# Optimization experiments

Hardware: AMD Instinct MI355X
Metric: run time of the kernel (lower is better)

The kernel has to match this reference:

```python
import jax, jax.numpy as jnp
import numpy as np

N = 100_000   # nodes
E = 1_600_000 # edges (avg degree 16)
D = 128       # input_dim
H = 128       # hidden_dim
G = 64        # graphs in batch
C = 2         # num_classes


def setup_inputs() -> dict:
    key = jax.random.key(0)
    ks = jax.random.split(key, 16)
    x = jax.random.normal(ks[0], (N, D), dtype=jnp.float32)
    edge_index = jax.random.randint(ks[1], (2, E), 0, N, dtype=jnp.int32)
    batch = jnp.sort(jax.random.randint(ks[2], (N,), 0, G, dtype=jnp.int32))
    def lin(k, fin, fout):
        s = 1.0 / np.sqrt(fin)
        kw, kb = jax.random.split(k)
        W = jax.random.uniform(kw, (fin, fout), jnp.float32, -s, s)
        b = jax.random.uniform(kb, (fout,), jnp.float32, -s, s)
        return W, b
    W0, b0 = lin(ks[3], D, H)
    W1, b1 = lin(ks[4], H, H)
    W2, b2 = lin(ks[5], H, H)
    Wc1, bc1 = lin(ks[6], 2 * H, H)
    Wc2, bc2 = lin(ks[7], H, C)
    return dict(x=x, edge_index=edge_index, batch=batch,
                W0=W0, b0=b0, W1=W1, b1=b1, W2=W2, b2=b2,
                Wc1=Wc1, bc1=bc1, Wc2=Wc2, bc2=bc2)


def _gcn_layer(x, W, b, src, dst, dinv):
    # GCNConv with self-loops and symmetric normalization:
    # out_i = sum_{j->i} d_j^{-1/2} d_i^{-1/2} (x_j W) + d_i^{-1} (x_i W) + b
    h = x @ W                                   # [N, H]
    coef = dinv[src] * dinv[dst]                # [E]
    agg = jax.ops.segment_sum(h[src] * coef[:, None], dst, num_segments=N)
    return agg + h * (dinv * dinv)[:, None] + b


def reference(x, edge_index, batch, W0, b0, W1, b1, W2, b2, Wc1, bc1, Wc2, bc2):
    src, dst = edge_index[0], edge_index[1]
    # degree with self-loops (in-degree on target nodes + 1)
    deg = jax.ops.segment_sum(jnp.ones((E,), jnp.float32), dst, num_segments=N) + 1.0
    dinv = jax.lax.rsqrt(deg)
    for W, b in ((W0, b0), (W1, b1), (W2, b2)):
        x = jax.nn.relu(_gcn_layer(x, W, b, src, dst, dinv))
        # dropout: inference mode -> identity
    # global mean pool per graph
    sums = jax.ops.segment_sum(x, batch, num_segments=G)            # [G, H]
    cnt = jax.ops.segment_sum(jnp.ones((N,), jnp.float32), batch, num_segments=G)
    pooled = sums / jnp.maximum(cnt, 1.0)[:, None]
    combined = jnp.concatenate([pooled, pooled], axis=1)            # [G, 2H]
    hcls = jax.nn.relu(combined @ Wc1 + bc1)
    return hcls @ Wc2 + bc2                                         # [G, C]
```

## Files before the change

kernel.cpp:

```cpp
#include <hip/hip_runtime.h>

#define HDIM 128
#define GCOUNT 64
#define CHUNK 8192

__device__ __forceinline__ float bfl(unsigned u) { return __uint_as_float(u << 16); }
__device__ __forceinline__ float bfh(unsigned u) { return __uint_as_float(u & 0xffff0000u); }
__device__ __forceinline__ unsigned short f2bf(float f) {
  unsigned u = __float_as_uint(f);
  unsigned r = (u + 0x7fffu + ((u >> 16) & 1u)) >> 16;
  return (unsigned short)r;
}
__device__ __forceinline__ unsigned pk2(float a, float b) {
  return (unsigned)f2bf(a) | ((unsigned)f2bf(b) << 16);
}

typedef __attribute__((ext_vector_type(8))) short short8;
typedef __attribute__((ext_vector_type(4))) float f32x4;

__device__ __forceinline__ unsigned qb(float v, float rinv) {
  int q = (int)rintf(v * rinv);
  return (unsigned)(q & 0xff);
}


__global__ void mega1(const float* __restrict__ W0, const float* __restrict__ W1,
                      const float* __restrict__ W2,
                      unsigned short* __restrict__ h0, unsigned short* __restrict__ l0,
                      unsigned short* __restrict__ h1, unsigned short* __restrict__ l1,
                      unsigned short* __restrict__ h2, unsigned short* __restrict__ l2,
                      float* __restrict__ pooled, float* __restrict__ gcnt, int pz,
                      const int* __restrict__ dst, int E, int G, int NB1,
                      int* __restrict__ gcount,
                      const float* __restrict__ x, uint2* __restrict__ S,
                      float* __restrict__ cs_base, int n) {
  __shared__ int hist[512];
  int b = blockIdx.x, t = threadIdx.x;
  if (b < 192) {
    int w = b >> 6;
    int idx = (b & 63) * 256 + t;
    const float* W = (w == 0) ? W0 : (w == 1) ? W1 : W2;
    unsigned short* hi = (w == 0) ? h0 : (w == 1) ? h1 : h2;
    unsigned short* lo = (w == 0) ? l0 : (w == 1) ? l1 : l2;
    int k = idx >> 7, nn = idx & 127;
    float wv = W[idx];
    unsigned short h = f2bf(wv);
    float hf = __uint_as_float((unsigned)h << 16);
    unsigned short l = f2bf(wv - hf);
    hi[nn * 128 + k] = h;
    lo[nn * 128 + k] = l;
  } else if (b < 192 + pz) {
    int i = (b - 192) * 256 + t;
    if (i < GCOUNT * HDIM) pooled[i] = 0.f;
    else if (i - GCOUNT * HDIM < GCOUNT) gcnt[i - GCOUNT * HDIM] = 0.f;
  } else if (b < 192 + pz + G) {
    int blk = b - 192 - pz;
    for (int i = t; i < NB1; i += 256) hist[i] = 0;
    __syncthreads();
    int base = blk * CHUNK;
    for (int i = t; i < CHUNK; i += 256) {
      int e = base + i;
      if (e < E) atomicAdd(&hist[dst[e] >> 8], 1);
    }
    __syncthreads();
    for (int i = t; i < NB1; i += 256) gcount[i * G + blk] = hist[i];
  } else {
    int idx = (b - 192 - pz - G) * 16 + (t >> 4);
    int l = t & 15;
    int ridx = min(idx, n - 1);
    float4 f0 = ((const float4*)x)[(size_t)ridx * 32 + l * 2];
    float4 f1 = ((const float4*)x)[(size_t)ridx * 32 + l * 2 + 1];
    float v0 = f0.x, v1 = f0.y, v2 = f0.z, v3 = f0.w;
    float v4 = f1.x, v5 = f1.y, v6 = f1.z, v7 = f1.w;
    float mx = fmaxf(fmaxf(fmaxf(fabsf(v0), fabsf(v1)), fmaxf(fabsf(v2), fabsf(v3))),
                     fmaxf(fmaxf(fabsf(v4), fabsf(v5)), fmaxf(fabsf(v6), fabsf(v7))));
    mx = fmaxf(mx, __shfl_xor(mx, 1));
    mx = fmaxf(mx, __shfl_xor(mx, 2));
    mx = fmaxf(mx, __shfl_xor(mx, 4));
    mx = fmaxf(mx, __shfl_xor(mx, 8));
    float c = mx * (1.0f / 127.0f);
    float rinv = (mx > 0.f) ? 127.0f / mx : 0.f;
    if (idx < n) {
      unsigned lo = qb(v0, rinv) | (qb(v1, rinv) << 8) | (qb(v2, rinv) << 16) | (qb(v3, rinv) << 24);
      unsigned hi = qb(v4, rinv) | (qb(v5, rinv) << 8) | (qb(v6, rinv) << 16) | (qb(v7, rinv) << 24);
      S[(size_t)idx * 16 + l] = make_uint2(lo, hi);
      if (l == 0) cs_base[idx] = c;
    }
  }
}


__global__ void scanA(int* __restrict__ g, int* __restrict__ bsum, int M) {
  __shared__ int sh[256];
  int t = threadIdx.x;
  int i = blockIdx.x * 256 + t;
  int v = (i < M) ? g[i] : 0;
  sh[t] = v;
  __syncthreads();
  for (int off = 1; off < 256; off <<= 1) {
    int u = (t >= off) ? sh[t - off] : 0;
    __syncthreads();
    sh[t] += u;
    __syncthreads();
  }
  if (i < M) g[i] = sh[t] - v;
  if (t == 255) bsum[blockIdx.x] = sh[255];
}

__global__ void scanB(int* __restrict__ g, const int* __restrict__ bsum, int nb, int M) {
  __shared__ int sh[512];
  int t = threadIdx.x;
  sh[t] = (t < nb) ? bsum[t] : 0;
  __syncthreads();
  for (int off = 1; off < 512; off <<= 1) {
    int u = (t >= off) ? sh[t - off] : 0;
    __syncthreads();
    sh[t] += u;
    __syncthreads();
  }
  #pragma unroll
  for (int k = 0; k < 2; k++) {
    int i = blockIdx.x * 1024 + k * 512 + t;
    if (i < M) {
      int j = i >> 8;
      if (j) g[i] += sh[j - 1];
    }
  }
}


__global__ void rs_scatter(const int* __restrict__ src, const int* __restrict__ dst,
                           const int* __restrict__ gscan, int E, int G, int NB1,
                           uint2* __restrict__ sp) {
  __shared__ int run[512];
  int blk = blockIdx.x, t = threadIdx.x;
  for (int i = t; i < NB1; i += 256) run[i] = gscan[i * G + blk];
  __syncthreads();
  int base = blk * CHUNK;
  for (int i = t; i < CHUNK; i += 256) {
    int e = base + i;
    if (e < E) {
      int d = dst[e];
      int pos = atomicAdd(&run[d >> 8], 1);
      sp[pos] = make_uint2((unsigned)d, (unsigned)src[e]);
    }
  }
}


__global__ void csr_fine(const uint2* __restrict__ sp, const int* __restrict__ gscan,
                         int E, int G, int NB1,
                         int* __restrict__ rowp, int* __restrict__ colv,
                         float* __restrict__ dinv, const float* __restrict__ cs_base,
                         float* __restrict__ cs, int n) {
  __shared__ int hist[256];
  __shared__ int scn[256];
  __shared__ int run2[256];
  int hb = blockIdx.x, t = threadIdx.x;
  int O = gscan[hb * G];
  int Oe = (hb == NB1 - 1) ? E : gscan[(hb + 1) * G];
  hist[t] = 0;
  __syncthreads();
  for (int e = O + t; e < Oe; e += 256) atomicAdd(&hist[sp[e].x & 255], 1);
  __syncthreads();
  int v = hist[t];
  scn[t] = v;
  __syncthreads();
  for (int off = 1; off < 256; off <<= 1) {
    int u = (t >= off) ? scn[t - off] : 0;
    __syncthreads();
    scn[t] += u;
    __syncthreads();
  }
  int excl = scn[t] - v;
  run2[t] = O + excl;
  int d = (hb << 8) + t;
  rowp[d] = O + excl;
  if (d < n) {
    float dv = rsqrtf((float)v + 1.0f);
    dinv[d] = dv;
    cs[d] = cs_base[d] * dv;
  }
  if (hb == NB1 - 1 && t == 0) rowp[n] = E;
  __syncthreads();
  for (int e = O + t; e < Oe; e += 256) {
    uint2 p = sp[e];
    int pos = atomicAdd(&run2[p.x & 255], 1);
    colv[pos] = (int)p.y;
  }
}


__device__ __forceinline__ void acc8(uint2 v, float c, float* a) {
  int xx = (int)v.x, yy = (int)v.y;
  a[0] += c * (float)(signed char)(xx);
  a[1] += c * (float)(signed char)(xx >> 8);
  a[2] += c * (float)(signed char)(xx >> 16);
  a[3] += c * (float)(xx >> 24);
  a[4] += c * (float)(signed char)(yy);
  a[5] += c * (float)(signed char)(yy >> 8);
  a[6] += c * (float)(signed char)(yy >> 16);
  a[7] += c * (float)(yy >> 24);
}

__global__ void agg_i8(const uint2* __restrict__ S, const float* __restrict__ cs,
                       const float* __restrict__ dinv,
                       const int* __restrict__ rowp, const int* __restrict__ col,
                       uint4* __restrict__ OUT, int n) {
  int g = (blockIdx.x * blockDim.x + threadIdx.x) >> 4;
  int lane = threadIdx.x & 15;
  if (g >= n) return;
  float a[8];
  {
    uint2 q = S[(size_t)g * 16 + lane];
    float c = cs[g];
    int xx = (int)q.x, yy = (int)q.y;
    a[0] = c * (float)(signed char)(xx);
    a[1] = c * (float)(signed char)(xx >> 8);
    a[2] = c * (float)(signed char)(xx >> 16);
    a[3] = c * (float)(xx >> 24);
    a[4] = c * (float)(signed char)(yy);
    a[5] = c * (float)(signed char)(yy >> 8);
    a[6] = c * (float)(signed char)(yy >> 16);
    a[7] = c * (float)(yy >> 24);
  }
  int e0 = rowp[g], e1 = rowp[g + 1];
  int e = e0;
  for (; e + 3 < e1; e += 4) {
    int s0 = col[e], s1 = col[e + 1], s2 = col[e + 2], s3 = col[e + 3];
    uint2 q0 = S[(size_t)s0 * 16 + lane];
    uint2 q1 = S[(size_t)s1 * 16 + lane];
    uint2 q2 = S[(size_t)s2 * 16 + lane];
    uint2 q3 = S[(size_t)s3 * 16 + lane];
    float c0 = cs[s0], c1 = cs[s1], c2 = cs[s2], c3 = cs[s3];
    acc8(q0, c0, a); acc8(q1, c1, a); acc8(q2, c2, a); acc8(q3, c3, a);
  }
  for (; e < e1; e++) {
    int s = col[e];
    uint2 q = S[(size_t)s * 16 + lane];
    acc8(q, cs[s], a);
  }
  float d = dinv[g];
  uint4 o;
  o.x = pk2(a[0] * d, a[1] * d); o.y = pk2(a[2] * d, a[3] * d);
  o.z = pk2(a[4] * d, a[5] * d); o.w = pk2(a[6] * d, a[7] * d);
  OUT[(size_t)g * 16 + lane] = o;
}


__global__ __launch_bounds__(256) void gemm_mfma_q8(
    const uint4* __restrict__ A, const uint4* __restrict__ WThi, const uint4* __restrict__ WTlo,
    const float* __restrict__ bias, const float* __restrict__ dinv,
    unsigned char* __restrict__ Sout, float* __restrict__ csout, int n) {
  __shared__ char smem[34816];
  __shared__ float Lc[64];
  uint4* Wl = (uint4*)smem;
  int t = threadIdx.x;
  int lane = t & 63, wv = t >> 6;
  int m = lane & 15, quad = lane >> 4;
  int block0 = blockIdx.x * 64;
  int arow = block0 + wv * 16 + m;
  uint4 av[4];
  #pragma unroll
  for (int kb = 0; kb < 4; kb++)
    av[kb] = (arow < n) ? A[(size_t)arow * 16 + kb * 4 + quad] : make_uint4(0, 0, 0, 0);
  f32x4 acc[8];
  #pragma unroll
  for (int i = 0; i < 8; i++) acc[i] = (f32x4){0.f, 0.f, 0.f, 0.f};

  #pragma unroll
  for (int i = 0; i < 8; i++) {
    int idx = t + i * 256;
    Wl[(idx >> 4) * 17 + (idx & 15)] = WThi[idx];
  }
  __syncthreads();
  #pragma unroll
  for (int kb = 0; kb < 4; kb++) {
    short8 af = __builtin_bit_cast(short8, av[kb]);
    #pragma unroll
    for (int nt = 0; nt < 8; nt++) {
      uint4 bh = Wl[(nt * 16 + m) * 17 + kb * 4 + quad];
      acc[nt] = __builtin_amdgcn_mfma_f32_16x16x32_bf16(af, __builtin_bit_cast(short8, bh), acc[nt], 0, 0, 0);
    }
  }
  __syncthreads();
  #pragma unroll
  for (int i = 0; i < 8; i++) {
    int idx = t + i * 256;
    Wl[(idx >> 4) * 17 + (idx & 15)] = WTlo[idx];
  }
  __syncthreads();
  #pragma unroll
  for (int kb = 0; kb < 4; kb++) {
    short8 af = __builtin_bit_cast(short8, av[kb]);
    #pragma unroll
    for (int nt = 0; nt < 8; nt++) {
      uint4 bl = Wl[(nt * 16 + m) * 17 + kb * 4 + quad];
      acc[nt] = __builtin_amdgcn_mfma_f32_16x16x32_bf16(af, __builtin_bit_cast(short8, bl), acc[nt], 0, 0, 0);
    }
  }
  __syncthreads();

  #pragma unroll
  for (int r = 0; r < 4; r++) {
    int lrow = wv * 16 + quad * 4 + r;
    int grow = block0 + lrow;
    float sc = (grow < n) ? dinv[grow] : 0.f;
    float v[8];
    float mx = 0.f;
    #pragma unroll
    for (int nt = 0; nt < 8; nt++) {
      v[nt] = fmaxf(acc[nt][r] + bias[nt * 16 + m], 0.f) * sc;
      mx = fmaxf(mx, v[nt]);
    }
    mx = fmaxf(mx, __shfl_xor(mx, 1));
    mx = fmaxf(mx, __shfl_xor(mx, 2));
    mx = fmaxf(mx, __shfl_xor(mx, 4));
    mx = fmaxf(mx, __shfl_xor(mx, 8));
    float c = mx * (1.0f / 127.0f);
    float rinv = (mx > 0.f) ? 127.0f / mx : 0.f;
    #pragma unroll
    for (int nt = 0; nt < 8; nt++) {
      smem[lrow * 144 + nt * 16 + m] = (char)(int)rintf(v[nt] * rinv);
    }
    if (m == 0) Lc[lrow] = c;
  }
  __syncthreads();
  for (int i = t; i < 512; i += 256) {
    int lrow = i >> 3, seg = i & 7;
    int grow = block0 + lrow;
    if (grow < n)
      ((uint4*)Sout)[(size_t)grow * 8 + seg] = *(const uint4*)&smem[lrow * 144 + seg * 16];
  }
  if (t < 64 && block0 + t < n) csout[block0 + t] = Lc[t];
}


__global__ __launch_bounds__(256) void gemm_mfma(
    const uint4* __restrict__ A, const uint4* __restrict__ WThi, const uint4* __restrict__ WTlo,
    const float* __restrict__ bias, unsigned short* __restrict__ Y, int n) {
  __shared__ char smem[34816];
  uint4* Wl = (uint4*)smem;
  int t = threadIdx.x;
  int lane = t & 63, wv = t >> 6;
  int m = lane & 15, quad = lane >> 4;
  int block0 = blockIdx.x * 64;
  int arow = block0 + wv * 16 + m;
  uint4 av[4];
  #pragma unroll
  for (int kb = 0; kb < 4; kb++)
    av[kb] = (arow < n) ? A[(size_t)arow * 16 + kb * 4 + quad] : make_uint4(0, 0, 0, 0);
  f32x4 acc[8];
  #pragma unroll
  for (int i = 0; i < 8; i++) acc[i] = (f32x4){0.f, 0.f, 0.f, 0.f};

  #pragma unroll
  for (int i = 0; i < 8; i++) {
    int idx = t + i * 256;
    Wl[(idx >> 4) * 17 + (idx & 15)] = WThi[idx];
  }
  __syncthreads();
  #pragma unroll
  for (int kb = 0; kb < 4; kb++) {
    short8 af = __builtin_bit_cast(short8, av[kb]);
    #pragma unroll
    for (int nt = 0; nt < 8; nt++) {
      uint4 bh = Wl[(nt * 16 + m) * 17 + kb * 4 + quad];
      acc[nt] = __builtin_amdgcn_mfma_f32_16x16x32_bf16(af, __builtin_bit_cast(short8, bh), acc[nt], 0, 0, 0);
    }
  }
  __syncthreads();
  #pragma unroll
  for (int i = 0; i < 8; i++) {
    int idx = t + i * 256;
    Wl[(idx >> 4) * 17 + (idx & 15)] = WTlo[idx];
  }
  __syncthreads();
  #pragma unroll
  for (int kb = 0; kb < 4; kb++) {
    short8 af = __builtin_bit_cast(short8, av[kb]);
    #pragma unroll
    for (int nt = 0; nt < 8; nt++) {
      uint4 bl = Wl[(nt * 16 + m) * 17 + kb * 4 + quad];
      acc[nt] = __builtin_amdgcn_mfma_f32_16x16x32_bf16(af, __builtin_bit_cast(short8, bl), acc[nt], 0, 0, 0);
    }
  }
  __syncthreads();

  unsigned short* Ls = (unsigned short*)smem;
  #pragma unroll
  for (int r = 0; r < 4; r++) {
    int lrow = wv * 16 + quad * 4 + r;
    #pragma unroll
    for (int nt = 0; nt < 8; nt++) {
      float v = fmaxf(acc[nt][r] + bias[nt * 16 + m], 0.f);
      Ls[lrow * 136 + nt * 16 + m] = f2bf(v);
    }
  }
  __syncthreads();
  for (int i = t; i < 1024; i += 256) {
    int lrow = i >> 4, seg = i & 15;
    int grow = block0 + lrow;
    if (grow < n)
      ((uint4*)Y)[(size_t)grow * 16 + seg] = *(const uint4*)&smem[lrow * 272 + seg * 16];
  }
}


__global__ void pool_kernel(const unsigned short* __restrict__ X, const int* __restrict__ batch,
                            float* __restrict__ pooled, float* __restrict__ gcnt, int n) {
  int t = threadIdx.x;
  int r0 = blockIdx.x * 64;
  if (r0 >= n) return;
  int r1 = min(r0 + 64, n);
  int g = batch[r0];
  float acc = 0.f, cl = 0.f;
  for (int r = r0; r < r1; r++) {
    int gr = batch[r];
    if (gr != g) {
      atomicAdd(&pooled[g * HDIM + t], acc);
      if (t == 0) atomicAdd(&gcnt[g], cl);
      acc = 0.f; cl = 0.f; g = gr;
    }
    acc += __uint_as_float((unsigned)X[(size_t)r * HDIM + t] << 16);
    cl += 1.f;
  }
  atomicAdd(&pooled[g * HDIM + t], acc);
  if (t == 0) atomicAdd(&gcnt[g], cl);
}


__global__ void cls_kernel(const float* __restrict__ pooled, const float* __restrict__ gcnt,
                           const float* __restrict__ Wc1, const float* __restrict__ bc1,
                           const float* __restrict__ Wc2, const float* __restrict__ bc2,
                           float* __restrict__ out) {
  __shared__ float p[HDIM];
  __shared__ float r0s[HDIM], r1s[HDIM];
  int g = blockIdx.x, t = threadIdx.x;
  float c = fmaxf(gcnt[g], 1.0f);
  p[t] = pooled[g * HDIM + t] / c;
  __syncthreads();
  float acc = bc1[t];
  for (int k = 0; k < HDIM; k++) {
    acc += p[k] * (Wc1[k * HDIM + t] + Wc1[(HDIM + k) * HDIM + t]);
  }
  float h = fmaxf(acc, 0.f);
  r0s[t] = h * Wc2[t * 2 + 0];
  r1s[t] = h * Wc2[t * 2 + 1];
  __syncthreads();
  for (int s2 = 64; s2 > 0; s2 >>= 1) {
    if (t < s2) { r0s[t] += r0s[t + s2]; r1s[t] += r1s[t + s2]; }
    __syncthreads();
  }
  if (t == 0) {
    out[g * 2 + 0] = r0s[0] + bc2[0];
    out[g * 2 + 1] = r1s[0] + bc2[1];
  }
}


extern "C" void kernel_launch(void* const* d_in, const int* in_sizes, int n_in,
                              void* d_out, int out_size, void* d_ws, size_t ws_size,
                              hipStream_t stream) {
  const float* x   = (const float*)d_in[0];
  const int*   ei  = (const int*)d_in[1];
  const int*   bat = (const int*)d_in[2];
  const float* W0  = (const float*)d_in[3];
  const float* b0  = (const float*)d_in[4];
  const float* W1  = (const float*)d_in[5];
  const float* b1  = (const float*)d_in[6];
  const float* W2  = (const float*)d_in[7];
  const float* b2  = (const float*)d_in[8];
  const float* Wc1 = (const float*)d_in[9];
  const float* bc1 = (const float*)d_in[10];
  const float* Wc2 = (const float*)d_in[11];
  const float* bc2 = (const float*)d_in[12];
  float* out = (float*)d_out;

  int N = in_sizes[0] / HDIM;
  int E = in_sizes[1] / 2;
  const int* src = ei;
  const int* dst = ei + E;

  int NB1 = (N + 255) >> 8;
  int G = (E + CHUNK - 1) / CHUNK;
  int M = NB1 * G;

  char* ws = (char*)d_ws;
  size_t off = 0;
  auto alloc = [&](size_t bytes) -> void* {
    void* p = (void*)(ws + off);
    off += (bytes + 511) & ~(size_t)511;
    return p;
  };
  unsigned char* Sa = (unsigned char*)alloc((size_t)N * HDIM * 2);
  unsigned char* Sb = Sa + (size_t)N * HDIM;
  unsigned short* H = (unsigned short*)Sa;
  unsigned short* Abuf = (unsigned short*)alloc((size_t)N * HDIM * 2);
  float* csa  = (float*)alloc((size_t)N * 4);
  float* csb  = (float*)alloc((size_t)N * 4);
  float* cs_base = (float*)alloc((size_t)N * 4);
  float* dinv = (float*)alloc((size_t)N * 4);
  int*   rowp = (int*)alloc((size_t)(NB1 * 256 + 2) * 4);
  int*   colv = (int*)alloc((size_t)E * 4);
  uint2* sp   = (uint2*)alloc((size_t)E * 8);
  float* pooled = (float*)alloc((size_t)GCOUNT * HDIM * 4);
  float* gcnt   = (float*)alloc((size_t)GCOUNT * 4);
  unsigned short* wt_hi[3], *wt_lo[3];
  for (int i = 0; i < 3; i++) {
    wt_hi[i] = (unsigned short*)alloc(HDIM * HDIM * 2);
    wt_lo[i] = (unsigned short*)alloc(HDIM * HDIM * 2);
  }
  int* gcount = (int*)alloc((size_t)(M + 2) * 4);
  int nbM = (M + 255) / 256;
  int* bsum = (int*)alloc((size_t)nbM * 4);

  int pz = (GCOUNT * HDIM + GCOUNT + 255) / 256;
  int psb = (N + 15) / 16;
  mega1<<<192 + pz + G + psb, 256, 0, stream>>>(W0, W1, W2,
      wt_hi[0], wt_lo[0], wt_hi[1], wt_lo[1], wt_hi[2], wt_lo[2],
      pooled, gcnt, pz, dst, E, G, NB1, gcount,
      x, (uint2*)Sa, cs_base, N);

  scanA<<<nbM, 256, 0, stream>>>(gcount, bsum, M);
  scanB<<<(M + 1023) / 1024, 512, 0, stream>>>(gcount, bsum, nbM, M);

  rs_scatter<<<G, 256, 0, stream>>>(src, dst, gcount, E, G, NB1, sp);
  csr_fine<<<NB1, 256, 0, stream>>>(sp, gcount, E, G, NB1, rowp, colv,
      dinv, cs_base, csa, N);

  int aggBlocks = (N + 15) / 16;
  int gemmBlocks = (N + 63) / 64;

  agg_i8<<<aggBlocks, 256, 0, stream>>>((const uint2*)Sa, csa, dinv, rowp, colv, (uint4*)Abuf, N);
  gemm_mfma_q8<<<gemmBlocks, 256, 0, stream>>>((const uint4*)Abuf, (const uint4*)wt_hi[0],
      (const uint4*)wt_lo[0], b0, dinv, Sb, csb, N);

  agg_i8<<<aggBlocks, 256, 0, stream>>>((const uint2*)Sb, csb, dinv, rowp, colv, (uint4*)Abuf, N);
  gemm_mfma_q8<<<gemmBlocks, 256, 0, stream>>>((const uint4*)Abuf, (const uint4*)wt_hi[1],
      (const uint4*)wt_lo[1], b1, dinv, Sa, csa, N);

  agg_i8<<<aggBlocks, 256, 0, stream>>>((const uint2*)Sa, csa, dinv, rowp, colv, (uint4*)Abuf, N);
  gemm_mfma<<<gemmBlocks, 256, 0, stream>>>((const uint4*)Abuf, (const uint4*)wt_hi[2],
      (const uint4*)wt_lo[2], b2, H, N);

  pool_kernel<<<(N + 63) / 64, 128, 0, stream>>>(H, bat, pooled, gcnt, N);
  cls_kernel<<<GCOUNT, HDIM, 0, stream>>>(pooled, gcnt, Wc1, bc1, Wc2, bc2, out);
}
```

Measured before the change: 383.2 us.

## Shrink edge chunks, widen scan and CSR blocks, unroll aggregation gather by 8

Cuts the edge chunk size from 8192 to 2048, giving four times as many histogram and scatter blocks, with fully unrolled per-thread loops. The two-level scan now uses 1024-thread blocks so fewer partial sums are needed despite the larger count matrix. The CSR fine-sort kernel uses 512 threads, and the int8 aggregation kernel adds an 8-way unrolled gather loop to keep more neighbour loads in flight. Each change aims to raise parallelism or memory-level parallelism in preprocessing and aggregation, at the cost of a larger count matrix to scan and higher register pressure in the aggregation kernel.

New measurement: 362.6 us. 5.4% less time.

```diff
diff --git a/kernel.cpp b/kernel.cpp
--- a/kernel.cpp
+++ b/kernel.cpp
@@ -2,7 +2,7 @@
 
 #define HDIM 128
 #define GCOUNT 64
-#define CHUNK 8192
+#define CHUNK 2048
 
 __device__ __forceinline__ float bfl(unsigned u) { return __uint_as_float(u << 16); }
 __device__ __forceinline__ float bfh(unsigned u) { return __uint_as_float(u & 0xffff0000u); }
@@ -58,8 +58,9 @@
     for (int i = t; i < NB1; i += 256) hist[i] = 0;
     __syncthreads();
     int base = blk * CHUNK;
-    for (int i = t; i < CHUNK; i += 256) {
-      int e = base + i;
+    #pragma unroll
+    for (int j = 0; j < CHUNK / 256; j++) {
+      int e = base + j * 256 + t;
       if (e < E) atomicAdd(&hist[dst[e] >> 8], 1);
     }
     __syncthreads();
@@ -91,38 +92,38 @@
 
 
 __global__ void scanA(int* __restrict__ g, int* __restrict__ bsum, int M) {
-  __shared__ int sh[256];
+  __shared__ int sh[1024];
   int t = threadIdx.x;
-  int i = blockIdx.x * 256 + t;
+  int i = blockIdx.x * 1024 + t;
   int v = (i < M) ? g[i] : 0;
   sh[t] = v;
   __syncthreads();
-  for (int off = 1; off < 256; off <<= 1) {
+  for (int off = 1; off < 1024; off <<= 1) {
     int u = (t >= off) ? sh[t - off] : 0;
     __syncthreads();
     sh[t] += u;
     __syncthreads();
   }
   if (i < M) g[i] = sh[t] - v;
-  if (t == 255) bsum[blockIdx.x] = sh[255];
+  if (t == 1023) bsum[blockIdx.x] = sh[1023];
 }
 
 __global__ void scanB(int* __restrict__ g, const int* __restrict__ bsum, int nb, int M) {
   __shared__ int sh[512];
   int t = threadIdx.x;
-  sh[t] = (t < nb) ? bsum[t] : 0;
+  if (t < 512) sh[t] = (t < nb) ? bsum[t] : 0;
   __syncthreads();
   for (int off = 1; off < 512; off <<= 1) {
-    int u = (t >= off) ? sh[t - off] : 0;
-    __syncthreads();
-    sh[t] += u;
+    int u = (t < 512 && t >= off) ? sh[t - off] : 0;
+    __syncthreads();
+    if (t < 512) sh[t] += u;
     __syncthreads();
   }
   #pragma unroll
   for (int k = 0; k < 2; k++) {
-    int i = blockIdx.x * 1024 + k * 512 + t;
+    int i = blockIdx.x * 2048 + k * 1024 + t;
     if (i < M) {
-      int j = i >> 8;
+      int j = i >> 10;
       if (j) g[i] += sh[j - 1];
     }
   }
@@ -137,8 +138,9 @@
   for (int i = t; i < NB1; i += 256) run[i] = gscan[i * G + blk];
   __syncthreads();
   int base = blk * CHUNK;
-  for (int i = t; i < CHUNK; i += 256) {
-    int e = base + i;
+  #pragma unroll
+  for (int j = 0; j < CHUNK / 256; j++) {
+    int e = base + j * 256 + t;
     if (e < E) {
       int d = dst[e];
       int pos = atomicAdd(&run[d >> 8], 1);
@@ -159,31 +161,33 @@
   int hb = blockIdx.x, t = threadIdx.x;
   int O = gscan[hb * G];
   int Oe = (hb == NB1 - 1) ? E : gscan[(hb + 1) * G];
-  hist[t] = 0;
-  __syncthreads();
-  for (int e = O + t; e < Oe; e += 256) atomicAdd(&hist[sp[e].x & 255], 1);
-  __syncthreads();
-  int v = hist[t];
-  scn[t] = v;
+  if (t < 256) hist[t] = 0;
+  __syncthreads();
+  for (int e = O + t; e < Oe; e += 512) atomicAdd(&hist[sp[e].x & 255], 1);
+  __syncthreads();
+  int v = 0;
+  if (t < 256) { v = hist[t]; scn[t] = v; }
   __syncthreads();
   for (int off = 1; off < 256; off <<= 1) {
-    int u = (t >= off) ? scn[t - off] : 0;
-    __syncthreads();
-    scn[t] += u;
-    __syncthreads();
-  }
-  int excl = scn[t] - v;
-  run2[t] = O + excl;
-  int d = (hb << 8) + t;
-  rowp[d] = O + excl;
-  if (d < n) {
-    float dv = rsqrtf((float)v + 1.0f);
-    dinv[d] = dv;
-    cs[d] = cs_base[d] * dv;
+    int u = (t < 256 && t >= off) ? scn[t - off] : 0;
+    __syncthreads();
+    if (t < 256) scn[t] += u;
+    __syncthreads();
+  }
+  if (t < 256) {
+    int excl = scn[t] - v;
+    run2[t] = O + excl;
+    int d = (hb << 8) + t;
+    rowp[d] = O + excl;
+    if (d < n) {
+      float dv = rsqrtf((float)v + 1.0f);
+      dinv[d] = dv;
+      cs[d] = cs_base[d] * dv;
+    }
   }
   if (hb == NB1 - 1 && t == 0) rowp[n] = E;
   __syncthreads();
-  for (int e = O + t; e < Oe; e += 256) {
+  for (int e = O + t; e < Oe; e += 512) {
     uint2 p = sp[e];
     int pos = atomicAdd(&run2[p.x & 255], 1);
     colv[pos] = (int)p.y;
@@ -226,6 +230,22 @@
   }
   int e0 = rowp[g], e1 = rowp[g + 1];
   int e = e0;
+  for (; e + 7 < e1; e += 8) {
+    int s0 = col[e],     s1 = col[e + 1], s2 = col[e + 2], s3 = col[e + 3];
+    int s4 = col[e + 4], s5 = col[e + 5], s6 = col[e + 6], s7 = col[e + 7];
+    uint2 q0 = S[(size_t)s0 * 16 + lane];
+    uint2 q1 = S[(size_t)s1 * 16 + lane];
+    uint2 q2 = S[(size_t)s2 * 16 + lane];
+    uint2 q3 = S[(size_t)s3 * 16 + lane];
+    uint2 q4 = S[(size_t)s4 * 16 + lane];
+    uint2 q5 = S[(size_t)s5 * 16 + lane];
+    uint2 q6 = S[(size_t)s6 * 16 + lane];
+    uint2 q7 = S[(size_t)s7 * 16 + lane];
+    float c0 = cs[s0], c1 = cs[s1], c2 = cs[s2], c3 = cs[s3];
+    float c4 = cs[s4], c5 = cs[s5], c6 = cs[s6], c7 = cs[s7];
+    acc8(q0, c0, a); acc8(q1, c1, a); acc8(q2, c2, a); acc8(q3, c3, a);
+    acc8(q4, c4, a); acc8(q5, c5, a); acc8(q6, c6, a); acc8(q7, c7, a);
+  }
   for (; e + 3 < e1; e += 4) {
     int s0 = col[e], s1 = col[e + 1], s2 = col[e + 2], s3 = col[e + 3];
     uint2 q0 = S[(size_t)s0 * 16 + lane];
@@ -512,7 +532,7 @@
     wt_lo[i] = (unsigned short*)alloc(HDIM * HDIM * 2);
   }
   int* gcount = (int*)alloc((size_t)(M + 2) * 4);
-  int nbM = (M + 255) / 256;
+  int nbM = (M + 1023) / 1024;
   int* bsum = (int*)alloc((size_t)nbM * 4);
 
   int pz = (GCOUNT * HDIM + GCOUNT + 255) / 256;
@@ -522,11 +542,11 @@
       pooled, gcnt, pz, dst, E, G, NB1, gcount,
       x, (uint2*)Sa, cs_base, N);
 
-  scanA<<<nbM, 256, 0, stream>>>(gcount, bsum, M);
-  scanB<<<(M + 1023) / 1024, 512, 0, stream>>>(gcount, bsum, nbM, M);
+  scanA<<<nbM, 1024, 0, stream>>>(gcount, bsum, M);
+  scanB<<<(M + 2047) / 2048, 1024, 0, stream>>>(gcount, bsum, nbM, M);
 
   rs_scatter<<<G, 256, 0, stream>>>(src, dst, gcount, E, G, NB1, sp);
-  csr_fine<<<NB1, 256, 0, stream>>>(sp, gcount, E, G, NB1, rowp, colv,
+  csr_fine<<<NB1, 512, 0, stream>>>(sp, gcount, E, G, NB1, rowp, colv,
       dinv, cs_base, csa, N);
 
   int aggBlocks = (N + 15) / 16;
```
